# Kernel tuning notes

Measured on AMD Instinct MI355X. Metric: run time of the kernel, lower is better.

## Reference

```python
import jax, jax.numpy as jnp
import numpy as np

IMAGE_SIZE = 960.0
ROI_SIZES = (3, 7, 11)
SCALE_DIMS = (22, 21, 21)  # output_dim=64 split across 3 scales (base 21 + remainder 1)
C, H, W, N = 64, 120, 120, 8192
HIDDEN = 128
GDIM = 64 // 4  # global context dim


def setup_inputs() -> dict:
    key = jax.random.key(0)
    ks = jax.random.split(key, 16)
    fm = jax.random.normal(ks[0], (1, C, H, W), dtype=jnp.float32)
    boxes = jax.random.uniform(ks[1], (N, 4), dtype=jnp.float32) * IMAGE_SIZE  # pixel coords
    inp = {"feature_maps": fm, "boxes": boxes}
    suffixes = ["a", "b", "c"]
    for i, (r, od) in enumerate(zip(ROI_SIZES, SCALE_DIMS)):
        fin = C * r * r
        inp[f"W1{suffixes[i]}"] = jax.random.normal(ks[2 + 4 * i], (HIDDEN, fin), dtype=jnp.float32) / np.sqrt(fin).astype(np.float32)
        inp[f"b1{suffixes[i]}"] = jnp.zeros((HIDDEN,), dtype=jnp.float32)
        inp[f"W2{suffixes[i]}"] = jax.random.normal(ks[3 + 4 * i], (od, HIDDEN), dtype=jnp.float32) / np.sqrt(HIDDEN).astype(np.float32)
        inp[f"b2{suffixes[i]}"] = jnp.zeros((od,), dtype=jnp.float32)
    inp["scale_w"] = jnp.ones((3,), dtype=jnp.float32)
    inp["Wg"] = jax.random.normal(ks[14], (GDIM, C), dtype=jnp.float32) / np.sqrt(C).astype(np.float32)
    inp["bg"] = jnp.zeros((GDIM,), dtype=jnp.float32)
    return inp


def _roi_sample(fm, boxes_n, r):
    """Bilinear grid_sample ROI extraction (align_corners=True, zero padding).
    fm: [C,H,W]; boxes_n: [N,4] normalized to [-1,1]. Returns [N,C,r,r]."""
    Cc, Hh, Ww = fm.shape
    t = jnp.linspace(0.0, 1.0, r)
    ty, tx = jnp.meshgrid(t, t, indexing="ij")  # [r,r]
    x1, y1, x2, y2 = boxes_n[:, 0], boxes_n[:, 1], boxes_n[:, 2], boxes_n[:, 3]
    gx = tx[None] * (x2 - x1)[:, None, None] + x1[:, None, None]  # [N,r,r]
    gy = ty[None] * (y2 - y1)[:, None, None] + y1[:, None, None]
    # align_corners=True mapping from [-1,1] to pixel index
    ix = (gx + 1.0) * 0.5 * (Ww - 1)
    iy = (gy + 1.0) * 0.5 * (Hh - 1)
    x0 = jnp.floor(ix)
    y0 = jnp.floor(iy)
    wx = ix - x0
    wy = iy - y0
    x0i = x0.astype(jnp.int32)
    y0i = y0.astype(jnp.int32)

    def gather(xi, yi):
        valid = (xi >= 0) & (xi <= Ww - 1) & (yi >= 0) & (yi <= Hh - 1)
        xc = jnp.clip(xi, 0, Ww - 1)
        yc = jnp.clip(yi, 0, Hh - 1)
        v = fm[:, yc, xc]  # [C,N,r,r]
        return v * valid[None].astype(fm.dtype)

    v00 = gather(x0i, y0i)
    v01 = gather(x0i + 1, y0i)
    v10 = gather(x0i, y0i + 1)
    v11 = gather(x0i + 1, y0i + 1)
    out = (v00 * (1 - wx) * (1 - wy) + v01 * wx * (1 - wy)
           + v10 * (1 - wx) * wy + v11 * wx * wy)  # [C,N,r,r]
    return jnp.transpose(out, (1, 0, 2, 3))  # [N,C,r,r]


def reference(feature_maps, boxes, W1a, b1a, W2a, b2a, W1b, b1b, W2b, b2b,
              W1c, b1c, W2c, b2c, scale_w, Wg, bg):
    fm = feature_maps[0]  # B==1
    boxes_n = boxes / IMAGE_SIZE * 2.0 - 1.0
    heads = [(W1a, b1a, W2a, b2a), (W1b, b1b, W2b, b2b), (W1c, b1c, W2c, b2c)]
    outs = []
    for i, r in enumerate(ROI_SIZES):
        roi = _roi_sample(fm, boxes_n, r)            # [N,C,r,r]
        x = roi.reshape(roi.shape[0], -1)            # flatten C-major like nn.Flatten
        W1, b1, W2, b2 = heads[i]
        h = jax.nn.relu(x @ W1.T + b1)
        o = jax.nn.relu(h @ W2.T + b2)               # dropout is identity at inference
        outs.append(o * scale_w[i])
    feats = jnp.concatenate(outs, axis=1)            # [N,64]
    gf = feature_maps.mean(axis=(2, 3))[0]           # adaptive avg pool -> [C]
    g = gf @ Wg.T + bg                               # [16]
    g = jnp.broadcast_to(g[None], (feats.shape[0], GDIM))
    return jnp.concatenate([feats[:, :64 - GDIM], g], axis=1)
```

## Files before the change

### kernel.cpp

```cpp
#include <hip/hip_runtime.h>
#include <hip/hip_fp16.h>
#include <stdint.h>

typedef float f4v __attribute__((ext_vector_type(4)));
typedef _Float16 h8v __attribute__((ext_vector_type(8)));

#define FMT_OFF   0
#define GF_OFF    1843200
#define W1P_OFF   1843712
#define W2T_OFF   4776448
#define PBUF_OFF  4801024

#define GLD(gp, lp) __builtin_amdgcn_global_load_lds( \
    (const __attribute__((address_space(1))) uint32_t*)(uintptr_t)(gp), \
    (__attribute__((address_space(3))) uint32_t*)(uintptr_t)(lp), 16, 0, 0)

__device__ __forceinline__ unsigned short f2hbits(float f) {
  __half h = __float2half_rn(f);
  union { __half h; unsigned short s; } u; u.h = h; return u.s;
}
__device__ __forceinline__ __half2 uh(unsigned int x) {
  union { unsigned int u; __half2 h; } v; v.u = x; return v.h;
}
__device__ __forceinline__ unsigned int hu(__half2 h) {
  union { __half2 h; unsigned int u; } v; v.h = h; return v.u;
}

__global__ void k_transpose(const float* __restrict__ fm, unsigned int* __restrict__ fmT32,
                            float* __restrict__ gf) {
  __shared__ float tile[64][65];
  int pixbase = blockIdx.x * 64, t = threadIdx.x;
  #pragma unroll
  for (int k = 0; k < 16; ++k) {
    int c = k * 4 + (t >> 6);
    tile[c][t & 63] = fm[c * 14400 + pixbase + (t & 63)];
  }
  __syncthreads();
  #pragma unroll
  for (int k = 0; k < 8; ++k) {
    int p = k * 8 + (t >> 5), i = t & 31;
    __half2 h = __floats2half2_rn(tile[2 * i][p], tile[2 * i + 1][p]);
    fmT32[(pixbase + p) * 32 + i] = hu(h);
  }
  int ch = t >> 2, seg = t & 3;
  float s = 0.f;
  #pragma unroll
  for (int j = 0; j < 16; ++j) s += tile[ch][seg * 16 + j];
  s += __shfl_xor(s, 1);
  s += __shfl_xor(s, 2);
  if (seg == 0) atomicAdd(&gf[ch], s);
}

__global__ void k_w1w2(const float* __restrict__ W1a, const float* __restrict__ W1b,
                       const float* __restrict__ W1c,
                       const float* __restrict__ W2a, const float* __restrict__ W2b,
                       const float* __restrict__ W2c,
                       unsigned short* __restrict__ w1p, unsigned short* __restrict__ w2t) {
  __shared__ float row[7744];
  int bi = blockIdx.x, t = threadIdx.x;
  if (bi >= 384) {
    int head = bi - 384;
    const float* W2 = head == 0 ? W2a : (head == 1 ? W2b : W2c);
    int od = head == 0 ? 22 : 21;
    #pragma unroll
    for (int it = 0; it < 16; ++it) {
      int e = it * 256 + t;
      int n = e >> 7, k = e & 127;
      float v = (n < od) ? W2[n * 128 + k] : 0.0f;
      w2t[head * 4096 + e] = f2hbits(v);
    }
    return;
  }
  int head = bi >> 7, j = bi & 127;
  const float* W1; int rr, base;
  if (head == 0)      { W1 = W1a; rr = 9;   base = 0; }
  else if (head == 1) { W1 = W1b; rr = 49;  base = 147456; }
  else                { W1 = W1c; rr = 121; base = 950272; }
  int fin = rr * 64;
  for (int idx = t; idx < fin; idx += 256) row[idx] = W1[j * fin + idx];
  __syncthreads();
  int swz = (j & 7) << 4;
  for (int idx = t; idx < fin; idx += 256) {
    int c = idx & 63, p = idx >> 6;
    int byteoff = base + p * 16384 + ((j * 128 + c * 2) ^ swz);
    w1p[byteoff >> 1] = f2hbits(row[c * rr + p]);
  }
}

__device__ __forceinline__ int2 mk_entry(float tx, float ty,
                                         float DX, float BX, float DY, float BY) {
  float ix = tx * DX + BX;
  float iy = ty * DY + BY;
  int x0 = min(max((int)floorf(ix), 0), 118);
  int y0 = min(max((int)floorf(iy), 0), 118);
  float wx = ix - (float)x0;
  float wy = iy - (float)y0;
  return make_int2((y0 * 120 + x0) * 128, (int)hu(__floats2half2_rn(wx, wy)));
}

__device__ __forceinline__ void sampleA(const char* __restrict__ fmT, int2 tv,
                                        int sbox, int scg, char* lds, int q) {
  __half2 wh = uh((unsigned int)tv.y);
  __half2 wx2 = __half2half2(__low2half(wh));
  __half2 wy2 = __half2half2(__high2half(wh));
  const char* src = fmT + tv.x + scg * 8;
  uint2 r00 = *(const uint2*)(src);
  uint2 r01 = *(const uint2*)(src + 128);
  uint2 r10 = *(const uint2*)(src + 15360);
  uint2 r11 = *(const uint2*)(src + 15488);
  __half2 a0 = uh(r00.x), a1 = uh(r00.y);
  __half2 b0 = uh(r01.x), b1 = uh(r01.y);
  __half2 c0 = uh(r10.x), c1 = uh(r10.y);
  __half2 d0 = uh(r11.x), d1 = uh(r11.y);
  __half2 t0 = __hfma2(wx2, __hsub2(b0, a0), a0);
  __half2 u0 = __hfma2(wx2, __hsub2(d0, c0), c0);
  __half2 v0 = __hfma2(wy2, __hsub2(u0, t0), t0);
  __half2 t1 = __hfma2(wx2, __hsub2(b1, a1), a1);
  __half2 u1 = __hfma2(wx2, __hsub2(d1, c1), c1);
  __half2 v1 = __hfma2(wy2, __hsub2(u1, t1), t1);
  int ab = q * 8192 + ((sbox * 128 + scg * 8) ^ ((sbox & 7) << 4));
  *(uint2*)(lds + ab) = make_uint2(hu(v0), hu(v1));
}

__global__ __launch_bounds__(512, 6) void k_main2(
    const char* __restrict__ fmT,
    const float* __restrict__ boxes,
    const char* __restrict__ w1p,
    unsigned short* __restrict__ pbuf)
{
  __shared__ __align__(16) char lds[51200];
  int bi = blockIdx.x;
  int head, tile64, split;
  if (bi < 512)      { head = 2; tile64 = bi >> 2;         split = bi & 3; }
  else if (bi < 768) { head = 1; tile64 = (bi - 512) >> 1; split = (bi - 512) & 1; }
  else               { head = 0; tile64 = bi - 768;        split = 0; }

  int psta, pcnt, w1base, pidx, R, rm; float invd;
  if (head == 2) {
    psta = split ? 31 + 30 * (split - 1) : 0; pcnt = split ? 30 : 31;
    w1base = 950272; pidx = tile64 * 4 + split; R = 11; rm = 5958; invd = 0.1f;
  } else if (head == 1) {
    psta = split * 25; pcnt = split ? 24 : 25;
    w1base = 147456; pidx = 512 + tile64 * 2 + split; R = 7; rm = 9363; invd = 0.166666667f;
  } else {
    psta = 0; pcnt = 9; w1base = 0; pidx = 768 + tile64; R = 3; rm = 21846; invd = 0.5f;
  }

  int tid = threadIdx.x;
  int w = tid >> 6, lane = tid & 63;
  int l15 = lane & 15, kgrp = lane >> 4;
  int kg = w >> 2, wc = w & 3;
  int boxbase = tile64 * 64;

  int eq = tid >> 6, ebox = tid & 63;
  float DX = 0.f, BX = 0.f, DY = 0.f, BY = 0.f;
  int px = 0, py = 0;
  if (tid < 128) {
    float4 bx = ((const float4*)boxes)[boxbase + ebox];
    const float sc2 = 119.0f / 960.0f;
    DX = (bx.z - bx.x) * sc2; BX = bx.x * sc2;
    DY = (bx.w - bx.y) * sc2; BY = bx.y * sc2;
    int p0 = psta + eq;
    py = (p0 * rm) >> 16;
    px = p0 - py * R;
    *(int2*)(lds + 49152 + (eq * 64 + ebox) * 8) =
        mk_entry((float)px * invd, (float)py * invd, DX, BX, DY, BY);
  }

  f4v acc[4][2];
  #pragma unroll
  for (int m = 0; m < 4; ++m)
    #pragma unroll
    for (int n = 0; n < 2; ++n) acc[m][n] = (f4v){0.f, 0.f, 0.f, 0.f};

  const char* w1g = w1p + w1base;
  int niter = (pcnt + 1) >> 1;
  __syncthreads();

  for (int it = 0; it < niter; ++it) {
    int p0 = psta + 2 * it;
    bool has1 = (2 * it + 1) < pcnt;
    int cur = it & 1, nxt = cur ^ 1;

    {
      const char* s0 = w1g + p0 * 16384 + w * 2048 + lane * 16;
      char* d0 = lds + 16384 + w * 2048;
      GLD(s0, d0); GLD(s0 + 1024, d0 + 1024);
      if (has1) {
        GLD(s0 + 16384, d0 + 16384); GLD(s0 + 17408, d0 + 17408);
      }
    }

    if (tid < 128) {
      px += 2; if (px >= R) { px -= R; ++py; }
      *(int2*)(lds + 49152 + nxt * 1024 + (eq * 64 + ebox) * 8) =
          mk_entry((float)px * invd, (float)py * invd, DX, BX, DY, BY);
    }

    {
      const char* eb = lds + 49152 + cur * 1024;
      int sb0 = tid >> 4, scg = tid & 15;
      #pragma unroll
      for (int u = 0; u < 4; ++u) {
        int rep = u & 1, q = u >> 1;
        if (q == 0 || has1) {
          int sbox = rep * 32 + sb0;
          int2 tv = *(const int2*)(eb + (q * 64 + sbox) * 8);
          sampleA(fmT, tv, sbox, scg, lds, q);
        }
      }
    }
    __syncthreads();

    if (kg == 0 || has1) {
      const char* abase = lds + kg * 8192;
      const char* bbase = lds + 16384 + kg * 16384;
      #pragma unroll
      for (int ks = 0; ks < 2; ++ks) {
        h8v bf[2];
        #pragma unroll
        for (int n = 0; n < 2; ++n) {
          int nrow = wc * 32 + n * 16 + l15;
          bf[n] = *(const h8v*)(bbase + ((nrow * 128 + ks * 64 + kgrp * 16) ^ ((nrow & 7) << 4)));
        }
        #pragma unroll
        for (int m = 0; m < 4; ++m) {
          int rrow = m * 16 + l15;
          h8v af = *(const h8v*)(abase + ((rrow * 128 + ks * 64 + kgrp * 16) ^ ((rrow & 7) << 4)));
          #pragma unroll
          for (int n = 0; n < 2; ++n)
            acc[m][n] = __builtin_amdgcn_mfma_f32_16x16x32_f16(af, bf[n], acc[m][n], 0, 0, 0);
        }
      }
    }
    __syncthreads();
  }

  if (kg == 1) {
    #pragma unroll
    for (int m = 0; m < 4; ++m)
      #pragma unroll
      for (int n = 0; n < 2; ++n)
        #pragma unroll
        for (int e = 0; e < 4; ++e) {
          int boxl = m * 16 + kgrp * 4 + e;
          int cnl = wc * 32 + n * 16 + l15;
          *(float*)(lds + (boxl * 128 + cnl) * 4) = acc[m][n][e];
        }
  }
  __syncthreads();
  if (kg == 0) {
    unsigned short* pdst = pbuf + pidx * 8192;
    #pragma unroll
    for (int m = 0; m < 4; ++m)
      #pragma unroll
      for (int n = 0; n < 2; ++n)
        #pragma unroll
        for (int e = 0; e < 4; ++e) {
          int boxl = m * 16 + kgrp * 4 + e;
          int cnl = wc * 32 + n * 16 + l15;
          float v = acc[m][n][e] + *(const float*)(lds + (boxl * 128 + cnl) * 4);
          pdst[boxl * 128 + cnl] = f2hbits(v);
        }
  }
}

__global__ __launch_bounds__(256) void k_combine(
    const unsigned short* __restrict__ pbuf,
    const unsigned short* __restrict__ w2t,
    const float* __restrict__ gf,
    const float* __restrict__ Wg, const float* __restrict__ bg,
    const float* __restrict__ b1a, const float* __restrict__ b1b, const float* __restrict__ b1c,
    const float* __restrict__ b2a, const float* __restrict__ b2b, const float* __restrict__ b2c,
    const float* __restrict__ scale_w,
    float* __restrict__ out)
{
  __shared__ __align__(16) char lds[8192 + 256];
  float* gv = (float*)(lds + 8192);
  int b = blockIdx.x, tid = threadIdx.x;
  int tile64 = b >> 1, rowoff = (b & 1) * 32;
  int boxbase = b * 32;
  int w = tid >> 6, lane = tid & 63, l15 = lane & 15, kgrp = lane >> 4;

  if (tid < 16) {
    float s = bg[tid];
    for (int c = 0; c < 64; ++c) s += gf[c] * (1.0f / 14400.0f) * Wg[tid * 64 + c];
    gv[tid] = s;
  }

  int row = tid >> 3, col0 = (tid & 7) * 16;
  const float* b1s[3] = {b1a, b1b, b1c};
  const float* b2s[3] = {b2a, b2b, b2c};

  #pragma unroll
  for (int h = 0; h < 3; ++h) {
    int S, pb, colbase, odh;
    if (h == 0)      { S = 1; pb = 768 + tile64;     colbase = 0;  odh = 22; }
    else if (h == 1) { S = 2; pb = 512 + tile64 * 2; colbase = 22; odh = 21; }
    else             { S = 4; pb = tile64 * 4;       colbase = 43; odh = 5; }

    float f[16];
    #pragma unroll
    for (int j = 0; j < 16; ++j) f[j] = 0.f;
    #pragma unroll
    for (int s = 0; s < 4; ++s) {
      if (s < S) {
        const unsigned short* src = pbuf + (pb + s) * 8192 + (rowoff + row) * 128 + col0;
        uint4 v0 = *(const uint4*)(src);
        uint4 v1 = *(const uint4*)(src + 8);
        unsigned int uu[8] = {v0.x, v0.y, v0.z, v0.w, v1.x, v1.y, v1.z, v1.w};
        #pragma unroll
        for (int k = 0; k < 8; ++k) {
          __half2 hv = uh(uu[k]);
          f[k * 2]     += __low2float(hv);
          f[k * 2 + 1] += __high2float(hv);
        }
      }
    }
    unsigned int pk[8];
    #pragma unroll
    for (int k = 0; k < 8; ++k) {
      float a  = fmaxf(f[2 * k]     + b1s[h][col0 + 2 * k],     0.f);
      float c2 = fmaxf(f[2 * k + 1] + b1s[h][col0 + 2 * k + 1], 0.f);
      pk[k] = hu(__floats2half2_rn(a, c2));
    }
    int swz = (row & 15) << 4;
    int a0 = (row * 256 + col0 * 2) ^ swz;
    int a1 = (row * 256 + col0 * 2 + 16) ^ swz;
    *(uint4*)(lds + a0) = make_uint4(pk[0], pk[1], pk[2], pk[3]);
    *(uint4*)(lds + a1) = make_uint4(pk[4], pk[5], pk[6], pk[7]);
    __syncthreads();

    {
      int m = w & 1, n2 = w >> 1;
      f4v a2 = (f4v){0.f, 0.f, 0.f, 0.f};
      int hrow = m * 16 + l15, drow = n2 * 16 + l15;
      #pragma unroll
      for (int ks = 0; ks < 4; ++ks) {
        h8v ha = *(const h8v*)(lds + ((hrow * 256 + ks * 64 + kgrp * 16) ^ ((hrow & 15) << 4)));
        h8v wb = *(const h8v*)((const char*)w2t + h * 8192 + drow * 256 + ks * 64 + kgrp * 16);
        a2 = __builtin_amdgcn_mfma_f32_16x16x32_f16(ha, wb, a2, 0, 0, 0);
      }
      if (drow < odh) {
        float scv = scale_w[h];
        float b2v = b2s[h][drow];
        #pragma unroll
        for (int e = 0; e < 4; ++e) {
          int box = boxbase + m * 16 + kgrp * 4 + e;
          out[box * 64 + colbase + drow] = fmaxf(a2[e] + b2v, 0.f) * scv;
        }
      }
    }
    __syncthreads();
  }

  {
    int i0 = tid * 2;
    #pragma unroll
    for (int j2 = 0; j2 < 2; ++j2) {
      int idx = i0 + j2;
      out[(boxbase + (idx >> 4)) * 64 + 48 + (idx & 15)] = gv[idx & 15];
    }
  }
}

extern "C" void kernel_launch(void* const* d_in, const int* in_sizes, int n_in,
                              void* d_out, int out_size, void* d_ws, size_t ws_size,
                              hipStream_t stream) {
  const float* fm      = (const float*)d_in[0];
  const float* boxes   = (const float*)d_in[1];
  const float* W1a     = (const float*)d_in[2];
  const float* b1a     = (const float*)d_in[3];
  const float* W2a     = (const float*)d_in[4];
  const float* b2a     = (const float*)d_in[5];
  const float* W1b     = (const float*)d_in[6];
  const float* b1b     = (const float*)d_in[7];
  const float* W2b     = (const float*)d_in[8];
  const float* b2b     = (const float*)d_in[9];
  const float* W1c     = (const float*)d_in[10];
  const float* b1c     = (const float*)d_in[11];
  const float* W2c     = (const float*)d_in[12];
  const float* b2c     = (const float*)d_in[13];
  const float* scale_w = (const float*)d_in[14];
  const float* Wg      = (const float*)d_in[15];
  const float* bg      = (const float*)d_in[16];

  char* ws = (char*)d_ws;
  unsigned int* fmT32 = (unsigned int*)(ws + FMT_OFF);
  float* gf           = (float*)(ws + GF_OFF);
  unsigned short* w1p = (unsigned short*)(ws + W1P_OFF);
  unsigned short* w2t = (unsigned short*)(ws + W2T_OFF);
  unsigned short* pbuf= (unsigned short*)(ws + PBUF_OFF);
  float* out          = (float*)d_out;

  hipMemsetAsync(gf, 0, 256, stream);
  k_transpose<<<225, 256, 0, stream>>>(fm, fmT32, gf);
  k_w1w2<<<387, 256, 0, stream>>>(W1a, W1b, W1c, W2a, W2b, W2c, w1p, w2t);
  k_main2<<<896, 512, 0, stream>>>((const char*)ws + FMT_OFF, boxes,
                                   (const char*)ws + W1P_OFF, pbuf);
  k_combine<<<256, 256, 0, stream>>>(pbuf, w2t, gf, Wg, bg,
                                     b1a, b1b, b1c, b2a, b2b, b2c, scale_w, out);
}
```

Before: 180.9 us.

## Use 128-box tiles with register-prefetched bilinear gathers and double-buffered W1

The main kernel now handles 128 boxes per block instead of 64. It uses half as many blocks and drops the two-way K-split and its LDS reduction. Each iteration now processes one sample point, and the feature-map gathers and W1 global-to-LDS loads for the next point are issued before the current MFMA step, so their latency overlaps compute. Gathers use 16-byte loads. The cost is more registers (launch bounds go from 6 to 4 blocks per CU), fewer blocks for the GPU, and a larger partial buffer layout that the combine kernel must match.

```diff
diff --git a/kernel.cpp b/kernel.cpp
--- a/kernel.cpp
+++ b/kernel.cpp
@@ -98,31 +98,32 @@
   return make_int2((y0 * 120 + x0) * 128, (int)hu(__floats2half2_rn(wx, wy)));
 }
 
-__device__ __forceinline__ void sampleA(const char* __restrict__ fmT, int2 tv,
-                                        int sbox, int scg, char* lds, int q) {
-  __half2 wh = uh((unsigned int)tv.y);
-  __half2 wx2 = __half2half2(__low2half(wh));
-  __half2 wy2 = __half2half2(__high2half(wh));
-  const char* src = fmT + tv.x + scg * 8;
-  uint2 r00 = *(const uint2*)(src);
-  uint2 r01 = *(const uint2*)(src + 128);
-  uint2 r10 = *(const uint2*)(src + 15360);
-  uint2 r11 = *(const uint2*)(src + 15488);
-  __half2 a0 = uh(r00.x), a1 = uh(r00.y);
-  __half2 b0 = uh(r01.x), b1 = uh(r01.y);
-  __half2 c0 = uh(r10.x), c1 = uh(r10.y);
-  __half2 d0 = uh(r11.x), d1 = uh(r11.y);
-  __half2 t0 = __hfma2(wx2, __hsub2(b0, a0), a0);
-  __half2 u0 = __hfma2(wx2, __hsub2(d0, c0), c0);
-  __half2 v0 = __hfma2(wy2, __hsub2(u0, t0), t0);
-  __half2 t1 = __hfma2(wx2, __hsub2(b1, a1), a1);
-  __half2 u1 = __hfma2(wx2, __hsub2(d1, c1), c1);
-  __half2 v1 = __hfma2(wy2, __hsub2(u1, t1), t1);
-  int ab = q * 8192 + ((sbox * 128 + scg * 8) ^ ((sbox & 7) << 4));
-  *(uint2*)(lds + ab) = make_uint2(hu(v0), hu(v1));
-}
-
-__global__ __launch_bounds__(512, 6) void k_main2(
+__device__ __forceinline__ unsigned lerp1(unsigned aa, unsigned bb, unsigned cc, unsigned dd,
+                                          __half2 wx2, __half2 wy2) {
+  __half2 a = uh(aa), b = uh(bb), c = uh(cc), d = uh(dd);
+  __half2 t = __hfma2(wx2, __hsub2(b, a), a);
+  __half2 u2 = __hfma2(wx2, __hsub2(d, c), c);
+  return hu(__hfma2(wy2, __hsub2(u2, t), t));
+}
+
+__device__ __forceinline__ void issue_pt(const char* lds, int ebOff, const char* __restrict__ fmT,
+                                         int sg, int scg8, uint4 cs[2][4],
+                                         __half2* wx2v, __half2* wy2v) {
+  #pragma unroll
+  for (int u = 0; u < 2; ++u) {
+    int2 e = *(const int2*)(lds + ebOff + (sg + u * 64) * 8);
+    __half2 wh = uh((unsigned)e.y);
+    wx2v[u] = __half2half2(__low2half(wh));
+    wy2v[u] = __half2half2(__high2half(wh));
+    const char* src = fmT + e.x + scg8 * 16;
+    cs[u][0] = *(const uint4*)(src);
+    cs[u][1] = *(const uint4*)(src + 128);
+    cs[u][2] = *(const uint4*)(src + 15360);
+    cs[u][3] = *(const uint4*)(src + 15488);
+  }
+}
+
+__global__ __launch_bounds__(512, 4) void k_main3(
     const char* __restrict__ fmT,
     const float* __restrict__ boxes,
     const char* __restrict__ w1p,
@@ -130,41 +131,31 @@
 {
   __shared__ __align__(16) char lds[51200];
   int bi = blockIdx.x;
-  int head, tile64, split;
-  if (bi < 512)      { head = 2; tile64 = bi >> 2;         split = bi & 3; }
-  else if (bi < 768) { head = 1; tile64 = (bi - 512) >> 1; split = (bi - 512) & 1; }
-  else               { head = 0; tile64 = bi - 768;        split = 0; }
-
-  int psta, pcnt, w1base, pidx, R, rm; float invd;
-  if (head == 2) {
-    psta = split ? 31 + 30 * (split - 1) : 0; pcnt = split ? 30 : 31;
-    w1base = 950272; pidx = tile64 * 4 + split; R = 11; rm = 5958; invd = 0.1f;
-  } else if (head == 1) {
-    psta = split * 25; pcnt = split ? 24 : 25;
-    w1base = 147456; pidx = 512 + tile64 * 2 + split; R = 7; rm = 9363; invd = 0.166666667f;
-  } else {
-    psta = 0; pcnt = 9; w1base = 0; pidx = 768 + tile64; R = 3; rm = 21846; invd = 0.5f;
-  }
+  int head, tile, split;
+  if (bi < 256)      { head = 2; tile = bi >> 2;         split = bi & 3; }
+  else if (bi < 384) { head = 1; tile = (bi - 256) >> 1; split = (bi - 256) & 1; }
+  else               { head = 0; tile = bi - 384;        split = 0; }
+
+  int psta, pcnt, w1base, R, rm; float invd;
+  if (head == 2)      { psta = split ? 31 + 30 * (split - 1) : 0; pcnt = split ? 30 : 31;
+                        w1base = 950272; R = 11; rm = 5958;  invd = 0.1f; }
+  else if (head == 1) { psta = split * 25; pcnt = 25 - split;
+                        w1base = 147456; R = 7;  rm = 9363;  invd = 0.166666667f; }
+  else                { psta = 0; pcnt = 9; w1base = 0; R = 3; rm = 21846; invd = 0.5f; }
 
   int tid = threadIdx.x;
   int w = tid >> 6, lane = tid & 63;
   int l15 = lane & 15, kgrp = lane >> 4;
-  int kg = w >> 2, wc = w & 3;
-  int boxbase = tile64 * 64;
-
-  int eq = tid >> 6, ebox = tid & 63;
+  int wm = w & 1, wc = w >> 1;
+  int sg = tid >> 3, scg8 = tid & 7;
+  int boxbase = tile * 128;
+
   float DX = 0.f, BX = 0.f, DY = 0.f, BY = 0.f;
-  int px = 0, py = 0;
   if (tid < 128) {
-    float4 bx = ((const float4*)boxes)[boxbase + ebox];
+    float4 bx = ((const float4*)boxes)[boxbase + tid];
     const float sc2 = 119.0f / 960.0f;
     DX = (bx.z - bx.x) * sc2; BX = bx.x * sc2;
     DY = (bx.w - bx.y) * sc2; BY = bx.y * sc2;
-    int p0 = psta + eq;
-    py = (p0 * rm) >> 16;
-    px = p0 - py * R;
-    *(int2*)(lds + 49152 + (eq * 64 + ebox) * 8) =
-        mk_entry((float)px * invd, (float)py * invd, DX, BX, DY, BY);
   }
 
   f4v acc[4][2];
@@ -174,95 +165,85 @@
     for (int n = 0; n < 2; ++n) acc[m][n] = (f4v){0.f, 0.f, 0.f, 0.f};
 
   const char* w1g = w1p + w1base;
-  int niter = (pcnt + 1) >> 1;
+  uint4 cs[2][4];
+  __half2 wx2v[2], wy2v[2];
+
+  if (tid < 128) {
+    #pragma unroll
+    for (int q = 0; q < 2; ++q) {
+      int p = psta + q;
+      int py = (p * rm) >> 16, px = p - py * R;
+      *(int2*)(lds + 49152 + q * 1024 + tid * 8) =
+          mk_entry((float)px * invd, (float)py * invd, DX, BX, DY, BY);
+    }
+  }
+  {
+    const char* s0 = w1g + psta * 16384 + w * 2048 + lane * 16;
+    char* d0 = lds + 16384 + w * 2048;
+    GLD(s0, d0); GLD(s0 + 1024, d0 + 1024);
+  }
   __syncthreads();
-
-  for (int it = 0; it < niter; ++it) {
-    int p0 = psta + 2 * it;
-    bool has1 = (2 * it + 1) < pcnt;
-    int cur = it & 1, nxt = cur ^ 1;
-
+  issue_pt(lds, 49152, fmT, sg, scg8, cs, wx2v, wy2v);
+
+  for (int t = 0; t < pcnt; ++t) {
+    int cur = t & 1, nxt = cur ^ 1;
+    bool more = (t + 1) < pcnt;
+
+    #pragma unroll
+    for (int u = 0; u < 2; ++u) {
+      int sbox = sg + u * 64;
+      uint4 r;
+      r.x = lerp1(cs[u][0].x, cs[u][1].x, cs[u][2].x, cs[u][3].x, wx2v[u], wy2v[u]);
+      r.y = lerp1(cs[u][0].y, cs[u][1].y, cs[u][2].y, cs[u][3].y, wx2v[u], wy2v[u]);
+      r.z = lerp1(cs[u][0].z, cs[u][1].z, cs[u][2].z, cs[u][3].z, wx2v[u], wy2v[u]);
+      r.w = lerp1(cs[u][0].w, cs[u][1].w, cs[u][2].w, cs[u][3].w, wx2v[u], wy2v[u]);
+      *(uint4*)(lds + ((sbox * 128 + scg8 * 16) ^ ((sbox & 7) << 4))) = r;
+    }
+    int2 ne;
+    if (tid < 128) {
+      int p = psta + min(t + 2, pcnt - 1);
+      int py = (p * rm) >> 16, px = p - py * R;
+      ne = mk_entry((float)px * invd, (float)py * invd, DX, BX, DY, BY);
+    }
+    __syncthreads();
+
+    if (tid < 128) *(int2*)(lds + 49152 + cur * 1024 + tid * 8) = ne;
+    if (more) {
+      const char* s0 = w1g + (psta + t + 1) * 16384 + w * 2048 + lane * 16;
+      char* d0 = lds + 16384 + nxt * 16384 + w * 2048;
+      GLD(s0, d0); GLD(s0 + 1024, d0 + 1024);
+      issue_pt(lds, 49152 + nxt * 1024, fmT, sg, scg8, cs, wx2v, wy2v);
+    }
     {
-      const char* s0 = w1g + p0 * 16384 + w * 2048 + lane * 16;
-      char* d0 = lds + 16384 + w * 2048;
-      GLD(s0, d0); GLD(s0 + 1024, d0 + 1024);
-      if (has1) {
-        GLD(s0 + 16384, d0 + 16384); GLD(s0 + 17408, d0 + 17408);
-      }
-    }
-
-    if (tid < 128) {
-      px += 2; if (px >= R) { px -= R; ++py; }
-      *(int2*)(lds + 49152 + nxt * 1024 + (eq * 64 + ebox) * 8) =
-          mk_entry((float)px * invd, (float)py * invd, DX, BX, DY, BY);
-    }
-
-    {
-      const char* eb = lds + 49152 + cur * 1024;
-      int sb0 = tid >> 4, scg = tid & 15;
-      #pragma unroll
-      for (int u = 0; u < 4; ++u) {
-        int rep = u & 1, q = u >> 1;
-        if (q == 0 || has1) {
-          int sbox = rep * 32 + sb0;
-          int2 tv = *(const int2*)(eb + (q * 64 + sbox) * 8);
-          sampleA(fmT, tv, sbox, scg, lds, q);
-        }
-      }
-    }
-    __syncthreads();
-
-    if (kg == 0 || has1) {
-      const char* abase = lds + kg * 8192;
-      const char* bbase = lds + 16384 + kg * 16384;
+      const char* bb = lds + 16384 + cur * 16384;
       #pragma unroll
       for (int ks = 0; ks < 2; ++ks) {
-        h8v bf[2];
-        #pragma unroll
-        for (int n = 0; n < 2; ++n) {
-          int nrow = wc * 32 + n * 16 + l15;
-          bf[n] = *(const h8v*)(bbase + ((nrow * 128 + ks * 64 + kgrp * 16) ^ ((nrow & 7) << 4)));
-        }
+        int n0 = wc * 32 + l15, n1 = n0 + 16;
+        h8v bf0 = *(const h8v*)(bb + ((n0 * 128 + ks * 64 + kgrp * 16) ^ ((n0 & 7) << 4)));
+        h8v bf1 = *(const h8v*)(bb + ((n1 * 128 + ks * 64 + kgrp * 16) ^ ((n1 & 7) << 4)));
         #pragma unroll
         for (int m = 0; m < 4; ++m) {
-          int rrow = m * 16 + l15;
-          h8v af = *(const h8v*)(abase + ((rrow * 128 + ks * 64 + kgrp * 16) ^ ((rrow & 7) << 4)));
-          #pragma unroll
-          for (int n = 0; n < 2; ++n)
-            acc[m][n] = __builtin_amdgcn_mfma_f32_16x16x32_f16(af, bf[n], acc[m][n], 0, 0, 0);
+          int rrow = wm * 64 + m * 16 + l15;
+          h8v af = *(const h8v*)(lds + ((rrow * 128 + ks * 64 + kgrp * 16) ^ ((rrow & 7) << 4)));
+          acc[m][0] = __builtin_amdgcn_mfma_f32_16x16x32_f16(af, bf0, acc[m][0], 0, 0, 0);
+          acc[m][1] = __builtin_amdgcn_mfma_f32_16x16x32_f16(af, bf1, acc[m][1], 0, 0, 0);
         }
       }
     }
     __syncthreads();
   }
 
-  if (kg == 1) {
-    #pragma unroll
-    for (int m = 0; m < 4; ++m)
+  unsigned short* pdst = pbuf + (size_t)bi * 16384;
+  #pragma unroll
+  for (int m = 0; m < 4; ++m)
+    #pragma unroll
+    for (int n = 0; n < 2; ++n)
       #pragma unroll
-      for (int n = 0; n < 2; ++n)
-        #pragma unroll
-        for (int e = 0; e < 4; ++e) {
-          int boxl = m * 16 + kgrp * 4 + e;
-          int cnl = wc * 32 + n * 16 + l15;
-          *(float*)(lds + (boxl * 128 + cnl) * 4) = acc[m][n][e];
-        }
-  }
-  __syncthreads();
-  if (kg == 0) {
-    unsigned short* pdst = pbuf + pidx * 8192;
-    #pragma unroll
-    for (int m = 0; m < 4; ++m)
-      #pragma unroll
-      for (int n = 0; n < 2; ++n)
-        #pragma unroll
-        for (int e = 0; e < 4; ++e) {
-          int boxl = m * 16 + kgrp * 4 + e;
-          int cnl = wc * 32 + n * 16 + l15;
-          float v = acc[m][n][e] + *(const float*)(lds + (boxl * 128 + cnl) * 4);
-          pdst[boxl * 128 + cnl] = f2hbits(v);
-        }
-  }
+      for (int e = 0; e < 4; ++e) {
+        int boxl = wm * 64 + m * 16 + kgrp * 4 + e;
+        int cnl = wc * 32 + n * 16 + l15;
+        pdst[boxl * 128 + cnl] = f2hbits(acc[m][n][e]);
+      }
 }
 
 __global__ __launch_bounds__(256) void k_combine(
@@ -278,7 +259,7 @@
   __shared__ __align__(16) char lds[8192 + 256];
   float* gv = (float*)(lds + 8192);
   int b = blockIdx.x, tid = threadIdx.x;
-  int tile64 = b >> 1, rowoff = (b & 1) * 32;
+  int tile = b >> 2, rowoff = (b & 3) * 32;
   int boxbase = b * 32;
   int w = tid >> 6, lane = tid & 63, l15 = lane & 15, kgrp = lane >> 4;
 
@@ -295,9 +276,9 @@
   #pragma unroll
   for (int h = 0; h < 3; ++h) {
     int S, pb, colbase, odh;
-    if (h == 0)      { S = 1; pb = 768 + tile64;     colbase = 0;  odh = 22; }
-    else if (h == 1) { S = 2; pb = 512 + tile64 * 2; colbase = 22; odh = 21; }
-    else             { S = 4; pb = tile64 * 4;       colbase = 43; odh = 5; }
+    if (h == 0)      { S = 1; pb = 384 + tile;     colbase = 0;  odh = 22; }
+    else if (h == 1) { S = 2; pb = 256 + tile * 2; colbase = 22; odh = 21; }
+    else             { S = 4; pb = tile * 4;       colbase = 43; odh = 5; }
 
     float f[16];
     #pragma unroll
@@ -305,7 +286,7 @@
     #pragma unroll
     for (int s = 0; s < 4; ++s) {
       if (s < S) {
-        const unsigned short* src = pbuf + (pb + s) * 8192 + (rowoff + row) * 128 + col0;
+        const unsigned short* src = pbuf + (size_t)(pb + s) * 16384 + (rowoff + row) * 128 + col0;
         uint4 v0 = *(const uint4*)(src);
         uint4 v1 = *(const uint4*)(src + 8);
         unsigned int uu[8] = {v0.x, v0.y, v0.z, v0.w, v1.x, v1.y, v1.z, v1.w};
@@ -396,7 +377,7 @@
   hipMemsetAsync(gf, 0, 256, stream);
   k_transpose<<<225, 256, 0, stream>>>(fm, fmT32, gf);
   k_w1w2<<<387, 256, 0, stream>>>(W1a, W1b, W1c, W2a, W2b, W2c, w1p, w2t);
-  k_main2<<<896, 512, 0, stream>>>((const char*)ws + FMT_OFF, boxes,
+  k_main3<<<448, 512, 0, stream>>>((const char*)ws + FMT_OFF, boxes,
                                    (const char*)ws + W1P_OFF, pbuf);
   k_combine<<<256, 256, 0, stream>>>(pbuf, w2t, gf, Wg, bg,
                                      b1a, b1b, b1c, b2a, b2b, b2c, scale_w, out);
```

New measurement: 167.0 us. 7.7% less time.
